# Optimization experiments

Hardware: AMD Instinct MI355X
Metric: run time of the kernel (lower is better)

## Reference

```python
import jax, jax.numpy as jnp
import numpy as np

B, N, C, H = 2, 2048, 256, 8
HD = C // H  # 32


def _pairwise_sq_dist(x, y):
    # x,y: [B,N,3] -> [B,N,N] squared euclidean distance
    x2 = jnp.sum(x * x, axis=-1)  # [B,N]
    y2 = jnp.sum(y * y, axis=-1)  # [B,N]
    xy = jnp.einsum('bnd,bmd->bnm', x, y)
    return x2[:, :, None] + y2[:, None, :] - 2.0 * xy


def setup_inputs() -> dict:
    key = jax.random.key(0)
    ks = jax.random.split(key, 12)
    s = 0.02
    return {
        'feature': jax.random.normal(ks[0], (B, N, C), jnp.float32),
        'points': jax.random.normal(ks[1], (B, N, 3), jnp.float32),
        'Wq': jax.random.normal(ks[2], (C, H * HD), jnp.float32) * s,
        'bq': jnp.zeros((H * HD,), jnp.float32),
        'Wk': jax.random.normal(ks[3], (C, H * HD), jnp.float32) * s,
        'bk': jnp.zeros((H * HD,), jnp.float32),
        'Wv': jax.random.normal(ks[4], (C, H * HD), jnp.float32) * s,
        'bv': jnp.zeros((H * HD,), jnp.float32),
        'Wo': jax.random.normal(ks[5], (H * HD, C), jnp.float32) * s,
        'bo': jnp.zeros((C,), jnp.float32),
        'ln_g': jnp.ones((C,), jnp.float32),
        'ln_b': jnp.zeros((C,), jnp.float32),
    }


def reference(feature, points, Wq, bq, Wk, bk, Wv, bv, Wo, bo, ln_g, ln_b):
    xyz = points[..., 0:3]
    dist = _pairwise_sq_dist(xyz, xyz)  # [B,N,N] geometric bias

    q = (feature @ Wq + bq).reshape(B, N, H, HD)
    k = (feature @ Wk + bk).reshape(B, N, H, HD)
    v = (feature @ Wv + bv).reshape(B, N, H, HD)

    # distance-biased multi-head attention (Geoglobal_FPT)
    logits = jnp.einsum('bnhd,bmhd->bhnm', q, k) / jnp.sqrt(jnp.float32(HD))
    logits = logits - dist[:, None, :, :]  # closer points attend more
    attn = jax.nn.softmax(logits, axis=-1)
    out = jnp.einsum('bhnm,bmhd->bnhd', attn, v).reshape(B, N, H * HD)
    out = out @ Wo + bo

    # residual + post-LayerNorm
    f = feature + out
    mu = jnp.mean(f, axis=-1, keepdims=True)
    var = jnp.mean(jnp.square(f - mu), axis=-1, keepdims=True)
    f = (f - mu) * jax.lax.rsqrt(var + 1e-5) * ln_g + ln_b
    return f
```

## Files before the change

### kernel.cpp

```cpp
#include <hip/hip_runtime.h>
#include <hip/hip_bf16.h>

#define B_ 2
#define N_ 2048
#define C_ 256
#define H_ 8
#define HD_ 32

typedef __bf16 bhalf;
typedef bhalf bhalf8 __attribute__((ext_vector_type(8)));
typedef bhalf bhalf4 __attribute__((ext_vector_type(4)));
typedef float floatx4 __attribute__((ext_vector_type(4)));
typedef short short4v __attribute__((ext_vector_type(4)));

__device__ __forceinline__ floatx4 mfma16x16x16bf16(bhalf4 a, bhalf4 b, floatx4 c) {
#if __has_builtin(__builtin_amdgcn_mfma_f32_16x16x16_bf16)
    return __builtin_amdgcn_mfma_f32_16x16x16_bf16(a, b, c, 0, 0, 0);
#else
    return __builtin_amdgcn_mfma_f32_16x16x16bf16_1k(
        __builtin_bit_cast(short4v, a), __builtin_bit_cast(short4v, b), c, 0, 0, 0);
#endif
}

__global__ __launch_bounds__(256) void prep_w(
    const float* __restrict__ Wq, const float* __restrict__ Wk,
    const float* __restrict__ Wv, const float* __restrict__ Wo,
    bhalf* __restrict__ Wtb)
{
    __shared__ float T[64][65];
    const float* W = blockIdx.y == 0 ? Wq : (blockIdx.y == 1 ? Wk : (blockIdx.y == 2 ? Wv : Wo));
    bhalf* dst = Wtb + (size_t)blockIdx.y * (C_ * C_);
    const int kt = (blockIdx.x >> 2) * 64, nt = (blockIdx.x & 3) * 64;
    const int t = threadIdx.x;
    const int c4 = (t & 15) * 4;
#pragma unroll
    for (int i = 0; i < 4; ++i) {
        const int r = (t >> 4) + i * 16;
        const float4 w = *(const float4*)&W[(kt + r) * C_ + nt + c4];
        T[r][c4 + 0] = w.x; T[r][c4 + 1] = w.y; T[r][c4 + 2] = w.z; T[r][c4 + 3] = w.w;
    }
    __syncthreads();
#pragma unroll
    for (int i = 0; i < 4; ++i) {
        const int n = (t >> 4) + i * 16;
        bhalf4 o;
        o[0] = (bhalf)T[c4 + 0][n]; o[1] = (bhalf)T[c4 + 1][n];
        o[2] = (bhalf)T[c4 + 2][n]; o[3] = (bhalf)T[c4 + 3][n];
        *(bhalf4*)&dst[(nt + n) * C_ + kt + c4] = o;
    }
}

__global__ __launch_bounds__(256) void prep_ext(
    const float* __restrict__ pts, bhalf* __restrict__ qext, bhalf* __restrict__ kext)
{
    const int i = blockIdx.x * 256 + threadIdx.x;
    const float x = pts[i * 3 + 0], y = pts[i * 3 + 1], z = pts[i * 3 + 2];
    const float nn = x * x + y * y + z * z;
    const bhalf hi = (bhalf)nn;
    const bhalf lo = (bhalf)(nn - (float)hi);
    bhalf8 qe, ke;
    qe[0] = (bhalf)(2.f * x); qe[1] = (bhalf)(2.f * y); qe[2] = (bhalf)(2.f * z);
    qe[3] = (bhalf)(-(float)hi); qe[4] = (bhalf)(-(float)lo);
    qe[5] = (bhalf)1.f; qe[6] = (bhalf)1.f; qe[7] = (bhalf)0.f;
    ke[0] = (bhalf)x; ke[1] = (bhalf)y; ke[2] = (bhalf)z;
    ke[3] = (bhalf)1.f; ke[4] = (bhalf)1.f;
    ke[5] = (bhalf)(-(float)hi); ke[6] = (bhalf)(-(float)lo); ke[7] = (bhalf)0.f;
    *(bhalf8*)&qext[(size_t)i * 8] = qe;
    *(bhalf8*)&kext[(size_t)i * 8] = ke;
}

__global__ __launch_bounds__(256) void qkv_gemm(
    const float* __restrict__ feat, const bhalf* __restrict__ Wtb,
    const float* __restrict__ bq, const float* __restrict__ bk,
    const float* __restrict__ bv,
    bhalf* __restrict__ qs, bhalf* __restrict__ kg, bhalf* __restrict__ vt)
{
    __shared__ __align__(16) bhalf Alds[64][72];
    __shared__ __align__(16) bhalf Blds[64][72];

    const int tid = threadIdx.x;
    const int wave = tid >> 6, lane = tid & 63;
    const int quad = lane >> 4, l16 = lane & 15;
    const int m0 = blockIdx.x * 64;
    const int which = blockIdx.y >> 2;
    const int n0 = (blockIdx.y & 3) * 64;
    const bhalf* Wt = Wtb + (size_t)which * (C_ * C_);
    const float* bias = which == 0 ? bq : (which == 1 ? bk : bv);

    const floatx4 zacc = {0.f, 0.f, 0.f, 0.f};
    floatx4 acc[4];
#pragma unroll
    for (int f = 0; f < 4; ++f) acc[f] = zacc;

    const int ar = tid >> 2, aseg = tid & 3;

    for (int kc = 0; kc < C_; kc += 64) {
        __syncthreads();
        {
            const float* fp = &feat[(m0 + ar) * C_ + kc + aseg * 16];
            const float4 a0 = *(const float4*)(fp);
            const float4 a1 = *(const float4*)(fp + 4);
            const float4 a2 = *(const float4*)(fp + 8);
            const float4 a3 = *(const float4*)(fp + 12);
            bhalf8 v0, v1;
            v0[0] = (bhalf)a0.x; v0[1] = (bhalf)a0.y; v0[2] = (bhalf)a0.z; v0[3] = (bhalf)a0.w;
            v0[4] = (bhalf)a1.x; v0[5] = (bhalf)a1.y; v0[6] = (bhalf)a1.z; v0[7] = (bhalf)a1.w;
            v1[0] = (bhalf)a2.x; v1[1] = (bhalf)a2.y; v1[2] = (bhalf)a2.z; v1[3] = (bhalf)a2.w;
            v1[4] = (bhalf)a3.x; v1[5] = (bhalf)a3.y; v1[6] = (bhalf)a3.z; v1[7] = (bhalf)a3.w;
            *(bhalf8*)&Alds[ar][aseg * 16] = v0;
            *(bhalf8*)&Alds[ar][aseg * 16 + 8] = v1;
            const bhalf* wp = &Wt[(n0 + ar) * C_ + kc + aseg * 16];
            *(bhalf8*)&Blds[ar][aseg * 16] = *(const bhalf8*)(wp);
            *(bhalf8*)&Blds[ar][aseg * 16 + 8] = *(const bhalf8*)(wp + 8);
        }
        __syncthreads();
        const bhalf8 af0 = *(const bhalf8*)&Alds[wave * 16 + l16][quad * 8];
        const bhalf8 af1 = *(const bhalf8*)&Alds[wave * 16 + l16][32 + quad * 8];
#pragma unroll
        for (int f = 0; f < 4; ++f) {
            const bhalf8 b0 = *(const bhalf8*)&Blds[f * 16 + l16][quad * 8];
            const bhalf8 b1 = *(const bhalf8*)&Blds[f * 16 + l16][32 + quad * 8];
            acc[f] = __builtin_amdgcn_mfma_f32_16x16x32_bf16(af0, b0, acc[f], 0, 0, 0);
            acc[f] = __builtin_amdgcn_mfma_f32_16x16x32_bf16(af1, b1, acc[f], 0, 0, 0);
        }
    }

    const float scale = 0.17677669529663687f;
#pragma unroll
    for (int f = 0; f < 4; ++f) {
        const int cg = n0 + f * 16 + l16;
        const float bi = bias[cg];
        const int hh = cg >> 5, dd = cg & 31;
#pragma unroll
        for (int r = 0; r < 4; ++r) {
            const int m = m0 + wave * 16 + quad * 4 + r;
            const int bb = m >> 11, nn = m & (N_ - 1);
            const float val = acc[f][r] + bi;
            if (which == 0) {
                qs[((size_t)(bb * H_ + hh) * N_ + nn) * HD_ + dd] = (bhalf)(val * scale);
            } else if (which == 1) {
                kg[((size_t)(bb * H_ + hh) * N_ + nn) * HD_ + dd] = (bhalf)val;
            } else {
                vt[(((size_t)(bb * H_ + hh) * (N_ / 64) + (nn >> 6)) * HD_ + dd) * 64 + (nn & 63)] = (bhalf)val;
            }
        }
    }
}

__global__ __launch_bounds__(256) void attn_kernel(
    const bhalf* __restrict__ qs, const bhalf* __restrict__ kg,
    const bhalf* __restrict__ vt, const bhalf* __restrict__ qext,
    const bhalf* __restrict__ kext,
    bhalf* __restrict__ po, float* __restrict__ pl, int spbits)
{
    __shared__ __align__(16) bhalf Ks[64][40];
    __shared__ __align__(16) bhalf Vts[32][72];

    const int tid = threadIdx.x;
    const int wave = tid >> 6, lane = tid & 63;
    const int quad = lane >> 4, l16 = lane & 15;
    const int n0 = blockIdx.x * 64;
    const int h = blockIdx.y;
    const int sp = blockIdx.z & ((1 << spbits) - 1);
    const int b = blockIdx.z >> spbits;
    const int bh = b * H_ + h;

    const int qrow = n0 + wave * 16 + l16;
    const bhalf8 bq_ = *(const bhalf8*)&qs[((size_t)bh * N_ + qrow) * HD_ + quad * 8];
    bhalf8 zv8;
#pragma unroll
    for (int j = 0; j < 8; ++j) zv8[j] = (bhalf)0.f;
    const bhalf8 bqe = (quad == 0)
        ? *(const bhalf8*)&qext[(size_t)(b * N_ + qrow) * 8] : zv8;

    const floatx4 zacc = {0.f, 0.f, 0.f, 0.f};
    floatx4 o0 = zacc, o1 = zacc;
    float ls = 0.f;

    const int skey = tid >> 2, sseg = tid & 3;
    const int vd = tid >> 3, vks = tid & 7;
    const int iters = (N_ >> spbits) / 64;
    const int mbase = sp * (N_ >> spbits);

    for (int it = 0; it < iters; ++it) {
        const int m0 = mbase + it * 64;
        __syncthreads();
        *(bhalf8*)&Ks[skey][sseg * 8] =
            *(const bhalf8*)&kg[((size_t)bh * N_ + m0 + skey) * HD_ + sseg * 8];
        *(bhalf8*)&Vts[vd][vks * 8] =
            *(const bhalf8*)&vt[(((size_t)bh * (N_ / 64) + (m0 >> 6)) * HD_ + vd) * 64 + vks * 8];
        __syncthreads();

#pragma unroll
        for (int mt = 0; mt < 4; ++mt) {
            const bhalf8 ak_ = *(const bhalf8*)&Ks[mt * 16 + l16][quad * 8];
            floatx4 st = __builtin_amdgcn_mfma_f32_16x16x32_bf16(ak_, bq_, zacc, 0, 0, 0);
            const bhalf8 ake = (quad == 0)
                ? *(const bhalf8*)&kext[(size_t)(b * N_ + m0 + mt * 16 + l16) * 8] : zv8;
            st = __builtin_amdgcn_mfma_f32_16x16x32_bf16(ake, bqe, st, 0, 0, 0);
            bhalf4 pt;
#pragma unroll
            for (int r = 0; r < 4; ++r) {
                const float p = __expf(st[r]);
                ls += p;
                pt[r] = (bhalf)p;
            }
            const bhalf4 av0 = *(const bhalf4*)&Vts[l16][mt * 16 + quad * 4];
            const bhalf4 av1 = *(const bhalf4*)&Vts[16 + l16][mt * 16 + quad * 4];
            o0 = mfma16x16x16bf16(av0, pt, o0);
            o1 = mfma16x16x16bf16(av1, pt, o1);
        }
    }

    ls += __shfl_xor(ls, 16);
    ls += __shfl_xor(ls, 32);

    const size_t pobase = (size_t)sp * ((size_t)B_ * H_ * N_ * HD_) + (size_t)bh * N_ * HD_;
    bhalf4 w0, w1;
#pragma unroll
    for (int r = 0; r < 4; ++r) { w0[r] = (bhalf)o0[r]; w1[r] = (bhalf)o1[r]; }
    *(bhalf4*)&po[pobase + (size_t)qrow * HD_ + quad * 4] = w0;
    *(bhalf4*)&po[pobase + (size_t)qrow * HD_ + 16 + quad * 4] = w1;
    if (lane < 16)
        pl[(size_t)sp * (B_ * H_ * N_) + (size_t)bh * N_ + qrow] = ls;
}

__global__ __launch_bounds__(256) void outln_gemm(
    const bhalf* __restrict__ po, const float* __restrict__ pl,
    const bhalf* __restrict__ Wot, const float* __restrict__ bo,
    const float* __restrict__ feat, const float* __restrict__ g,
    const float* __restrict__ bb, float* __restrict__ out, int splits)
{
    __shared__ __align__(16) bhalf Alds[16][264];
    __shared__ __align__(16) bhalf Blds[256][40];
    __shared__ float rden[16][8];
    __shared__ float wsum[4][16][2];
    __shared__ float stats[16][2];

    const int tid = threadIdx.x;
    const int wave = tid >> 6, lane = tid & 63;
    const int quad = lane >> 4, l16 = lane & 15;
    const int row0 = blockIdx.x * 16;

    if (tid < 128) {
        const int m = tid >> 3, hh = tid & 7;
        const int grow = row0 + m;
        const int b = grow >> 11, n = grow & (N_ - 1);
        float den = 0.f;
        for (int sp = 0; sp < splits; ++sp)
            den += pl[(size_t)sp * (B_ * H_ * N_) + (size_t)(b * H_ + hh) * N_ + n];
        rden[m][hh] = 1.f / den;
    }
    __syncthreads();

    {
        const int m = tid >> 4, seg = tid & 15;
        const int hh = seg >> 1, d0 = (seg & 1) * 16;
        const int grow = row0 + m;
        const int b = grow >> 11, n = grow & (N_ - 1);
        const size_t idx = ((size_t)(b * H_ + hh) * N_ + n) * HD_ + d0;
        float num[16];
#pragma unroll
        for (int j = 0; j < 16; ++j) num[j] = 0.f;
        for (int sp = 0; sp < splits; ++sp) {
            const bhalf8 p0 = *(const bhalf8*)&po[(size_t)sp * ((size_t)B_ * H_ * N_ * HD_) + idx];
            const bhalf8 p1 = *(const bhalf8*)&po[(size_t)sp * ((size_t)B_ * H_ * N_ * HD_) + idx + 8];
#pragma unroll
            for (int j = 0; j < 8; ++j) { num[j] += (float)p0[j]; num[8 + j] += (float)p1[j]; }
        }
        const float r = rden[m][hh];
        bhalf8 a0, a1;
#pragma unroll
        for (int j = 0; j < 8; ++j) { a0[j] = (bhalf)(num[j] * r); a1[j] = (bhalf)(num[8 + j] * r); }
        *(bhalf8*)&Alds[m][seg * 16] = a0;
        *(bhalf8*)&Alds[m][seg * 16 + 8] = a1;
    }

    const floatx4 zacc = {0.f, 0.f, 0.f, 0.f};
    floatx4 acc[4];
#pragma unroll
    for (int f = 0; f < 4; ++f) acc[f] = zacc;

    for (int kc = 0; kc < C_; kc += 32) {
        __syncthreads();
        {
            const bhalf* wp = &Wot[tid * C_ + kc];
            *(bhalf8*)&Blds[tid][0]  = *(const bhalf8*)(wp);
            *(bhalf8*)&Blds[tid][8]  = *(const bhalf8*)(wp + 8);
            *(bhalf8*)&Blds[tid][16] = *(const bhalf8*)(wp + 16);
            *(bhalf8*)&Blds[tid][24] = *(const bhalf8*)(wp + 24);
        }
        __syncthreads();
        const bhalf8 af = *(const bhalf8*)&Alds[l16][kc + quad * 8];
#pragma unroll
        for (int f = 0; f < 4; ++f) {
            const bhalf8 bfr = *(const bhalf8*)&Blds[wave * 64 + f * 16 + l16][quad * 8];
            acc[f] = __builtin_amdgcn_mfma_f32_16x16x32_bf16(af, bfr, acc[f], 0, 0, 0);
        }
    }

    float fv[4][4];
    float s1[4] = {0.f, 0.f, 0.f, 0.f}, s2[4] = {0.f, 0.f, 0.f, 0.f};
#pragma unroll
    for (int f = 0; f < 4; ++f) {
        const int col = wave * 64 + f * 16 + l16;
        const float bic = bo[col];
#pragma unroll
        for (int r = 0; r < 4; ++r) {
            const int m = quad * 4 + r;
            const float x = acc[f][r] + bic + feat[(row0 + m) * C_ + col];
            fv[f][r] = x;
            s1[r] += x; s2[r] += x * x;
        }
    }
#pragma unroll
    for (int r = 0; r < 4; ++r) {
        for (int o = 1; o < 16; o <<= 1) {
            s1[r] += __shfl_xor(s1[r], o);
            s2[r] += __shfl_xor(s2[r], o);
        }
    }
    if (l16 == 0) {
#pragma unroll
        for (int r = 0; r < 4; ++r) {
            wsum[wave][quad * 4 + r][0] = s1[r];
            wsum[wave][quad * 4 + r][1] = s2[r];
        }
    }
    __syncthreads();
    if (tid < 16) {
        float a = 0.f, bsq = 0.f;
#pragma unroll
        for (int w = 0; w < 4; ++w) { a += wsum[w][tid][0]; bsq += wsum[w][tid][1]; }
        const float mu = a * (1.f / C_);
        const float var = bsq * (1.f / C_) - mu * mu;
        stats[tid][0] = mu;
        stats[tid][1] = rsqrtf(var + 1e-5f);
    }
    __syncthreads();
#pragma unroll
    for (int f = 0; f < 4; ++f) {
        const int col = wave * 64 + f * 16 + l16;
        const float gc = g[col], bc = bb[col];
#pragma unroll
        for (int r = 0; r < 4; ++r) {
            const int m = quad * 4 + r;
            out[(row0 + m) * C_ + col] = (fv[f][r] - stats[m][0]) * stats[m][1] * gc + bc;
        }
    }
}

extern "C" void kernel_launch(void* const* d_in, const int* in_sizes, int n_in,
                              void* d_out, int out_size, void* d_ws, size_t ws_size,
                              hipStream_t stream) {
    const float* feat = (const float*)d_in[0];
    const float* pts  = (const float*)d_in[1];
    const float* Wq   = (const float*)d_in[2];
    const float* bq   = (const float*)d_in[3];
    const float* Wk   = (const float*)d_in[4];
    const float* bk   = (const float*)d_in[5];
    const float* Wv   = (const float*)d_in[6];
    const float* bv   = (const float*)d_in[7];
    const float* Wo   = (const float*)d_in[8];
    const float* bo   = (const float*)d_in[9];
    const float* lng  = (const float*)d_in[10];
    const float* lnb  = (const float*)d_in[11];

    char* w = (char*)d_ws;
    bhalf* Wtb  = (bhalf*)(w);
    bhalf* qs   = (bhalf*)(w + 524288);
    bhalf* kg   = (bhalf*)(w + 2621440);
    bhalf* vtp  = (bhalf*)(w + 4718592);
    bhalf* qext = (bhalf*)(w + 6815744);
    bhalf* kext = (bhalf*)(w + 6881280);
    float* pl   = (float*)(w + 6946816);
    bhalf* po   = (bhalf*)(w + 7471104);

    const int spbits = (ws_size >= 15859712u) ? 2 : 1;
    const int splits = 1 << spbits;

    prep_w<<<dim3(16, 4), 256, 0, stream>>>(Wq, Wk, Wv, Wo, Wtb);
    prep_ext<<<B_ * N_ / 256, 256, 0, stream>>>(pts, qext, kext);
    qkv_gemm<<<dim3(B_ * N_ / 64, 12), 256, 0, stream>>>(
        feat, Wtb, bq, bk, bv, qs, kg, vtp);
    attn_kernel<<<dim3(N_ / 64, H_, B_ << spbits), 256, 0, stream>>>(
        qs, kg, vtp, qext, kext, po, pl, spbits);
    outln_gemm<<<B_ * N_ / 16, 256, 0, stream>>>(
        po, pl, Wtb + 3 * (C_ * C_), bo, feat, lng, lnb, (float*)d_out, splits);
}
```

Baseline: 132.3 us.

## Merge prep kernels, pre-convert features to bf16, double-buffer LDS in all GEMM loops

Folds the weight transpose, point-extension and a new feature fp32-to-bf16 conversion into one prep launch. The QKV GEMM now reads bf16 features, uses 32-row tiles for twice as many blocks, and double-buffers LDS with register prefetch. The attention and output GEMM loops get the same double-buffered prefetch, and attention stages kext in LDS instead of reading it from global memory per tile. This trades extra LDS and registers plus an extra feature buffer round trip for fewer launches and fewer barrier stalls.

```diff
diff --git a/kernel.cpp b/kernel.cpp
--- a/kernel.cpp
+++ b/kernel.cpp
@@ -22,118 +22,130 @@
 #endif
 }
 
-__global__ __launch_bounds__(256) void prep_w(
+__global__ __launch_bounds__(256) void prep_all(
     const float* __restrict__ Wq, const float* __restrict__ Wk,
     const float* __restrict__ Wv, const float* __restrict__ Wo,
-    bhalf* __restrict__ Wtb)
+    const float* __restrict__ pts, const float* __restrict__ feat,
+    bhalf* __restrict__ Wtb, bhalf* __restrict__ qext,
+    bhalf* __restrict__ kext, bhalf* __restrict__ fb)
 {
     __shared__ float T[64][65];
-    const float* W = blockIdx.y == 0 ? Wq : (blockIdx.y == 1 ? Wk : (blockIdx.y == 2 ? Wv : Wo));
-    bhalf* dst = Wtb + (size_t)blockIdx.y * (C_ * C_);
-    const int kt = (blockIdx.x >> 2) * 64, nt = (blockIdx.x & 3) * 64;
+    const int bx = blockIdx.x;
     const int t = threadIdx.x;
-    const int c4 = (t & 15) * 4;
-#pragma unroll
-    for (int i = 0; i < 4; ++i) {
-        const int r = (t >> 4) + i * 16;
-        const float4 w = *(const float4*)&W[(kt + r) * C_ + nt + c4];
-        T[r][c4 + 0] = w.x; T[r][c4 + 1] = w.y; T[r][c4 + 2] = w.z; T[r][c4 + 3] = w.w;
-    }
-    __syncthreads();
-#pragma unroll
-    for (int i = 0; i < 4; ++i) {
-        const int n = (t >> 4) + i * 16;
+    if (bx < 64) {
+        const int wsel = bx >> 4;
+        const float* W = wsel == 0 ? Wq : (wsel == 1 ? Wk : (wsel == 2 ? Wv : Wo));
+        bhalf* dst = Wtb + (size_t)wsel * (C_ * C_);
+        const int tile = bx & 15;
+        const int kt = (tile >> 2) * 64, nt = (tile & 3) * 64;
+        const int c4 = (t & 15) * 4;
+#pragma unroll
+        for (int i = 0; i < 4; ++i) {
+            const int r = (t >> 4) + i * 16;
+            const float4 w = *(const float4*)&W[(kt + r) * C_ + nt + c4];
+            T[r][c4 + 0] = w.x; T[r][c4 + 1] = w.y; T[r][c4 + 2] = w.z; T[r][c4 + 3] = w.w;
+        }
+        __syncthreads();
+#pragma unroll
+        for (int i = 0; i < 4; ++i) {
+            const int n = (t >> 4) + i * 16;
+            bhalf4 o;
+            o[0] = (bhalf)T[c4 + 0][n]; o[1] = (bhalf)T[c4 + 1][n];
+            o[2] = (bhalf)T[c4 + 2][n]; o[3] = (bhalf)T[c4 + 3][n];
+            *(bhalf4*)&dst[(nt + n) * C_ + kt + c4] = o;
+        }
+    } else if (bx < 80) {
+        const int i = (bx - 64) * 256 + t;
+        const float x = pts[i * 3 + 0], y = pts[i * 3 + 1], z = pts[i * 3 + 2];
+        const float nn = x * x + y * y + z * z;
+        const bhalf hi = (bhalf)nn;
+        const bhalf lo = (bhalf)(nn - (float)hi);
+        bhalf8 qe, ke;
+        qe[0] = (bhalf)(2.f * x); qe[1] = (bhalf)(2.f * y); qe[2] = (bhalf)(2.f * z);
+        qe[3] = (bhalf)(-(float)hi); qe[4] = (bhalf)(-(float)lo);
+        qe[5] = (bhalf)1.f; qe[6] = (bhalf)1.f; qe[7] = (bhalf)0.f;
+        ke[0] = (bhalf)x; ke[1] = (bhalf)y; ke[2] = (bhalf)z;
+        ke[3] = (bhalf)1.f; ke[4] = (bhalf)1.f;
+        ke[5] = (bhalf)(-(float)hi); ke[6] = (bhalf)(-(float)lo); ke[7] = (bhalf)0.f;
+        *(bhalf8*)&qext[(size_t)i * 8] = qe;
+        *(bhalf8*)&kext[(size_t)i * 8] = ke;
+    } else {
+        const int idx = ((bx - 80) * 256 + t) * 4;
+        const float4 f = *(const float4*)&feat[idx];
         bhalf4 o;
-        o[0] = (bhalf)T[c4 + 0][n]; o[1] = (bhalf)T[c4 + 1][n];
-        o[2] = (bhalf)T[c4 + 2][n]; o[3] = (bhalf)T[c4 + 3][n];
-        *(bhalf4*)&dst[(nt + n) * C_ + kt + c4] = o;
-    }
-}
-
-__global__ __launch_bounds__(256) void prep_ext(
-    const float* __restrict__ pts, bhalf* __restrict__ qext, bhalf* __restrict__ kext)
-{
-    const int i = blockIdx.x * 256 + threadIdx.x;
-    const float x = pts[i * 3 + 0], y = pts[i * 3 + 1], z = pts[i * 3 + 2];
-    const float nn = x * x + y * y + z * z;
-    const bhalf hi = (bhalf)nn;
-    const bhalf lo = (bhalf)(nn - (float)hi);
-    bhalf8 qe, ke;
-    qe[0] = (bhalf)(2.f * x); qe[1] = (bhalf)(2.f * y); qe[2] = (bhalf)(2.f * z);
-    qe[3] = (bhalf)(-(float)hi); qe[4] = (bhalf)(-(float)lo);
-    qe[5] = (bhalf)1.f; qe[6] = (bhalf)1.f; qe[7] = (bhalf)0.f;
-    ke[0] = (bhalf)x; ke[1] = (bhalf)y; ke[2] = (bhalf)z;
-    ke[3] = (bhalf)1.f; ke[4] = (bhalf)1.f;
-    ke[5] = (bhalf)(-(float)hi); ke[6] = (bhalf)(-(float)lo); ke[7] = (bhalf)0.f;
-    *(bhalf8*)&qext[(size_t)i * 8] = qe;
-    *(bhalf8*)&kext[(size_t)i * 8] = ke;
+        o[0] = (bhalf)f.x; o[1] = (bhalf)f.y; o[2] = (bhalf)f.z; o[3] = (bhalf)f.w;
+        *(bhalf4*)&fb[idx] = o;
+    }
 }
 
 __global__ __launch_bounds__(256) void qkv_gemm(
-    const float* __restrict__ feat, const bhalf* __restrict__ Wtb,
+    const bhalf* __restrict__ fb, const bhalf* __restrict__ Wtb,
     const float* __restrict__ bq, const float* __restrict__ bk,
     const float* __restrict__ bv,
     bhalf* __restrict__ qs, bhalf* __restrict__ kg, bhalf* __restrict__ vt)
 {
-    __shared__ __align__(16) bhalf Alds[64][72];
-    __shared__ __align__(16) bhalf Blds[64][72];
+    __shared__ __align__(16) bhalf Alds[2][32][72];
+    __shared__ __align__(16) bhalf Blds[2][64][72];
 
     const int tid = threadIdx.x;
     const int wave = tid >> 6, lane = tid & 63;
     const int quad = lane >> 4, l16 = lane & 15;
-    const int m0 = blockIdx.x * 64;
+    const int m0 = blockIdx.x * 32;
     const int which = blockIdx.y >> 2;
     const int n0 = (blockIdx.y & 3) * 64;
     const bhalf* Wt = Wtb + (size_t)which * (C_ * C_);
+    const int mw = (wave & 1) * 16;
+    const int cw = (wave >> 1) * 32;
+
+    const floatx4 zacc = {0.f, 0.f, 0.f, 0.f};
+    floatx4 acc[2] = {zacc, zacc};
+
+    const int arow = tid >> 3, aoff = (tid & 7) * 8;
+    const int brow = tid >> 2, boff = (tid & 3) * 16;
+
+    bhalf8 ra  = *(const bhalf8*)&fb[(m0 + arow) * C_ + aoff];
+    bhalf8 rb0 = *(const bhalf8*)&Wt[(n0 + brow) * C_ + boff];
+    bhalf8 rb1 = *(const bhalf8*)&Wt[(n0 + brow) * C_ + boff + 8];
+    *(bhalf8*)&Alds[0][arow][aoff] = ra;
+    *(bhalf8*)&Blds[0][brow][boff] = rb0;
+    *(bhalf8*)&Blds[0][brow][boff + 8] = rb1;
+
+    int cur = 0;
+    for (int kci = 0; kci < 4; ++kci) {
+        __syncthreads();
+        if (kci < 3) {
+            const int kc = (kci + 1) * 64;
+            ra  = *(const bhalf8*)&fb[(m0 + arow) * C_ + kc + aoff];
+            rb0 = *(const bhalf8*)&Wt[(n0 + brow) * C_ + kc + boff];
+            rb1 = *(const bhalf8*)&Wt[(n0 + brow) * C_ + kc + boff + 8];
+        }
+        const bhalf8 a0 = *(const bhalf8*)&Alds[cur][mw + l16][quad * 8];
+        const bhalf8 a1 = *(const bhalf8*)&Alds[cur][mw + l16][32 + quad * 8];
+#pragma unroll
+        for (int f = 0; f < 2; ++f) {
+            const bhalf8 b0 = *(const bhalf8*)&Blds[cur][cw + f * 16 + l16][quad * 8];
+            const bhalf8 b1 = *(const bhalf8*)&Blds[cur][cw + f * 16 + l16][32 + quad * 8];
+            acc[f] = __builtin_amdgcn_mfma_f32_16x16x32_bf16(a0, b0, acc[f], 0, 0, 0);
+            acc[f] = __builtin_amdgcn_mfma_f32_16x16x32_bf16(a1, b1, acc[f], 0, 0, 0);
+        }
+        if (kci < 3) {
+            *(bhalf8*)&Alds[cur ^ 1][arow][aoff] = ra;
+            *(bhalf8*)&Blds[cur ^ 1][brow][boff] = rb0;
+            *(bhalf8*)&Blds[cur ^ 1][brow][boff + 8] = rb1;
+        }
+        cur ^= 1;
+    }
+
+    const float scale = 0.17677669529663687f;
     const float* bias = which == 0 ? bq : (which == 1 ? bk : bv);
-
-    const floatx4 zacc = {0.f, 0.f, 0.f, 0.f};
-    floatx4 acc[4];
-#pragma unroll
-    for (int f = 0; f < 4; ++f) acc[f] = zacc;
-
-    const int ar = tid >> 2, aseg = tid & 3;
-
-    for (int kc = 0; kc < C_; kc += 64) {
-        __syncthreads();
-        {
-            const float* fp = &feat[(m0 + ar) * C_ + kc + aseg * 16];
-            const float4 a0 = *(const float4*)(fp);
-            const float4 a1 = *(const float4*)(fp + 4);
-            const float4 a2 = *(const float4*)(fp + 8);
-            const float4 a3 = *(const float4*)(fp + 12);
-            bhalf8 v0, v1;
-            v0[0] = (bhalf)a0.x; v0[1] = (bhalf)a0.y; v0[2] = (bhalf)a0.z; v0[3] = (bhalf)a0.w;
-            v0[4] = (bhalf)a1.x; v0[5] = (bhalf)a1.y; v0[6] = (bhalf)a1.z; v0[7] = (bhalf)a1.w;
-            v1[0] = (bhalf)a2.x; v1[1] = (bhalf)a2.y; v1[2] = (bhalf)a2.z; v1[3] = (bhalf)a2.w;
-            v1[4] = (bhalf)a3.x; v1[5] = (bhalf)a3.y; v1[6] = (bhalf)a3.z; v1[7] = (bhalf)a3.w;
-            *(bhalf8*)&Alds[ar][aseg * 16] = v0;
-            *(bhalf8*)&Alds[ar][aseg * 16 + 8] = v1;
-            const bhalf* wp = &Wt[(n0 + ar) * C_ + kc + aseg * 16];
-            *(bhalf8*)&Blds[ar][aseg * 16] = *(const bhalf8*)(wp);
-            *(bhalf8*)&Blds[ar][aseg * 16 + 8] = *(const bhalf8*)(wp + 8);
-        }
-        __syncthreads();
-        const bhalf8 af0 = *(const bhalf8*)&Alds[wave * 16 + l16][quad * 8];
-        const bhalf8 af1 = *(const bhalf8*)&Alds[wave * 16 + l16][32 + quad * 8];
-#pragma unroll
-        for (int f = 0; f < 4; ++f) {
-            const bhalf8 b0 = *(const bhalf8*)&Blds[f * 16 + l16][quad * 8];
-            const bhalf8 b1 = *(const bhalf8*)&Blds[f * 16 + l16][32 + quad * 8];
-            acc[f] = __builtin_amdgcn_mfma_f32_16x16x32_bf16(af0, b0, acc[f], 0, 0, 0);
-            acc[f] = __builtin_amdgcn_mfma_f32_16x16x32_bf16(af1, b1, acc[f], 0, 0, 0);
-        }
-    }
-
-    const float scale = 0.17677669529663687f;
-#pragma unroll
-    for (int f = 0; f < 4; ++f) {
-        const int cg = n0 + f * 16 + l16;
+#pragma unroll
+    for (int f = 0; f < 2; ++f) {
+        const int cg = n0 + cw + f * 16 + l16;
         const float bi = bias[cg];
         const int hh = cg >> 5, dd = cg & 31;
 #pragma unroll
         for (int r = 0; r < 4; ++r) {
-            const int m = m0 + wave * 16 + quad * 4 + r;
+            const int m = m0 + mw + quad * 4 + r;
             const int bb = m >> 11, nn = m & (N_ - 1);
             const float val = acc[f][r] + bi;
             if (which == 0) {
@@ -153,8 +165,9 @@
     const bhalf* __restrict__ kext,
     bhalf* __restrict__ po, float* __restrict__ pl, int spbits)
 {
-    __shared__ __align__(16) bhalf Ks[64][40];
-    __shared__ __align__(16) bhalf Vts[32][72];
+    __shared__ __align__(16) bhalf Ks[2][64][40];
+    __shared__ __align__(16) bhalf Vts[2][32][72];
+    __shared__ __align__(16) bhalf Kes[2][64][8];
 
     const int tid = threadIdx.x;
     const int wave = tid >> 6, lane = tid & 63;
@@ -179,24 +192,33 @@
 
     const int skey = tid >> 2, sseg = tid & 3;
     const int vd = tid >> 3, vks = tid & 7;
+    const int ekey = tid >> 1, eoff = (tid & 1) * 4;
     const int iters = (N_ >> spbits) / 64;
     const int mbase = sp * (N_ >> spbits);
 
+    bhalf8 rk = *(const bhalf8*)&kg[((size_t)bh * N_ + mbase + skey) * HD_ + sseg * 8];
+    bhalf8 rv = *(const bhalf8*)&vt[(((size_t)bh * (N_ / 64) + (mbase >> 6)) * HD_ + vd) * 64 + vks * 8];
+    bhalf4 re;
+    if (tid < 128) re = *(const bhalf4*)&kext[(size_t)(b * N_ + mbase + ekey) * 8 + eoff];
+    *(bhalf8*)&Ks[0][skey][sseg * 8] = rk;
+    *(bhalf8*)&Vts[0][vd][vks * 8] = rv;
+    if (tid < 128) *(bhalf4*)&Kes[0][ekey][eoff] = re;
+
+    int cur = 0;
     for (int it = 0; it < iters; ++it) {
-        const int m0 = mbase + it * 64;
         __syncthreads();
-        *(bhalf8*)&Ks[skey][sseg * 8] =
-            *(const bhalf8*)&kg[((size_t)bh * N_ + m0 + skey) * HD_ + sseg * 8];
-        *(bhalf8*)&Vts[vd][vks * 8] =
-            *(const bhalf8*)&vt[(((size_t)bh * (N_ / 64) + (m0 >> 6)) * HD_ + vd) * 64 + vks * 8];
-        __syncthreads();
-
+        if (it + 1 < iters) {
+            const int m1 = mbase + (it + 1) * 64;
+            rk = *(const bhalf8*)&kg[((size_t)bh * N_ + m1 + skey) * HD_ + sseg * 8];
+            rv = *(const bhalf8*)&vt[(((size_t)bh * (N_ / 64) + (m1 >> 6)) * HD_ + vd) * 64 + vks * 8];
+            if (tid < 128) re = *(const bhalf4*)&kext[(size_t)(b * N_ + m1 + ekey) * 8 + eoff];
+        }
 #pragma unroll
         for (int mt = 0; mt < 4; ++mt) {
-            const bhalf8 ak_ = *(const bhalf8*)&Ks[mt * 16 + l16][quad * 8];
+            const bhalf8 ak_ = *(const bhalf8*)&Ks[cur][mt * 16 + l16][quad * 8];
             floatx4 st = __builtin_amdgcn_mfma_f32_16x16x32_bf16(ak_, bq_, zacc, 0, 0, 0);
             const bhalf8 ake = (quad == 0)
-                ? *(const bhalf8*)&kext[(size_t)(b * N_ + m0 + mt * 16 + l16) * 8] : zv8;
+                ? *(const bhalf8*)&Kes[cur][mt * 16 + l16][0] : zv8;
             st = __builtin_amdgcn_mfma_f32_16x16x32_bf16(ake, bqe, st, 0, 0, 0);
             bhalf4 pt;
 #pragma unroll
@@ -205,11 +227,17 @@
                 ls += p;
                 pt[r] = (bhalf)p;
             }
-            const bhalf4 av0 = *(const bhalf4*)&Vts[l16][mt * 16 + quad * 4];
-            const bhalf4 av1 = *(const bhalf4*)&Vts[16 + l16][mt * 16 + quad * 4];
+            const bhalf4 av0 = *(const bhalf4*)&Vts[cur][l16][mt * 16 + quad * 4];
+            const bhalf4 av1 = *(const bhalf4*)&Vts[cur][16 + l16][mt * 16 + quad * 4];
             o0 = mfma16x16x16bf16(av0, pt, o0);
             o1 = mfma16x16x16bf16(av1, pt, o1);
         }
+        if (it + 1 < iters) {
+            *(bhalf8*)&Ks[cur ^ 1][skey][sseg * 8] = rk;
+            *(bhalf8*)&Vts[cur ^ 1][vd][vks * 8] = rv;
+            if (tid < 128) *(bhalf4*)&Kes[cur ^ 1][ekey][eoff] = re;
+        }
+        cur ^= 1;
     }
 
     ls += __shfl_xor(ls, 16);
@@ -232,7 +260,7 @@
     const float* __restrict__ bb, float* __restrict__ out, int splits)
 {
     __shared__ __align__(16) bhalf Alds[16][264];
-    __shared__ __align__(16) bhalf Blds[256][40];
+    __shared__ __align__(16) bhalf Blds[2][256][40];
     __shared__ float rden[16][8];
     __shared__ float wsum[4][16][2];
     __shared__ float stats[16][2];
@@ -281,22 +309,38 @@
 #pragma unroll
     for (int f = 0; f < 4; ++f) acc[f] = zacc;
 
-    for (int kc = 0; kc < C_; kc += 32) {
+    bhalf8 rb0 = *(const bhalf8*)&Wot[tid * C_ + 0];
+    bhalf8 rb1 = *(const bhalf8*)&Wot[tid * C_ + 8];
+    bhalf8 rb2 = *(const bhalf8*)&Wot[tid * C_ + 16];
+    bhalf8 rb3 = *(const bhalf8*)&Wot[tid * C_ + 24];
+    *(bhalf8*)&Blds[0][tid][0]  = rb0;
+    *(bhalf8*)&Blds[0][tid][8]  = rb1;
+    *(bhalf8*)&Blds[0][tid][16] = rb2;
+    *(bhalf8*)&Blds[0][tid][24] = rb3;
+
+    int cur = 0;
+    for (int kci = 0; kci < 8; ++kci) {
         __syncthreads();
-        {
-            const bhalf* wp = &Wot[tid * C_ + kc];
-            *(bhalf8*)&Blds[tid][0]  = *(const bhalf8*)(wp);
-            *(bhalf8*)&Blds[tid][8]  = *(const bhalf8*)(wp + 8);
-            *(bhalf8*)&Blds[tid][16] = *(const bhalf8*)(wp + 16);
-            *(bhalf8*)&Blds[tid][24] = *(const bhalf8*)(wp + 24);
-        }
-        __syncthreads();
-        const bhalf8 af = *(const bhalf8*)&Alds[l16][kc + quad * 8];
+        if (kci < 7) {
+            const bhalf* wp = &Wot[tid * C_ + (kci + 1) * 32];
+            rb0 = *(const bhalf8*)(wp);
+            rb1 = *(const bhalf8*)(wp + 8);
+            rb2 = *(const bhalf8*)(wp + 16);
+            rb3 = *(const bhalf8*)(wp + 24);
+        }
+        const bhalf8 af = *(const bhalf8*)&Alds[l16][kci * 32 + quad * 8];
 #pragma unroll
         for (int f = 0; f < 4; ++f) {
-            const bhalf8 bfr = *(const bhalf8*)&Blds[wave * 64 + f * 16 + l16][quad * 8];
+            const bhalf8 bfr = *(const bhalf8*)&Blds[cur][wave * 64 + f * 16 + l16][quad * 8];
             acc[f] = __builtin_amdgcn_mfma_f32_16x16x32_bf16(af, bfr, acc[f], 0, 0, 0);
         }
+        if (kci < 7) {
+            *(bhalf8*)&Blds[cur ^ 1][tid][0]  = rb0;
+            *(bhalf8*)&Blds[cur ^ 1][tid][8]  = rb1;
+            *(bhalf8*)&Blds[cur ^ 1][tid][16] = rb2;
+            *(bhalf8*)&Blds[cur ^ 1][tid][24] = rb3;
+        }
+        cur ^= 1;
     }
 
     float fv[4][4];
@@ -368,21 +412,22 @@
 
     char* w = (char*)d_ws;
     bhalf* Wtb  = (bhalf*)(w);
-    bhalf* qs   = (bhalf*)(w + 524288);
-    bhalf* kg   = (bhalf*)(w + 2621440);
-    bhalf* vtp  = (bhalf*)(w + 4718592);
-    bhalf* qext = (bhalf*)(w + 6815744);
-    bhalf* kext = (bhalf*)(w + 6881280);
-    float* pl   = (float*)(w + 6946816);
-    bhalf* po   = (bhalf*)(w + 7471104);
-
-    const int spbits = (ws_size >= 15859712u) ? 2 : 1;
+    bhalf* fb   = (bhalf*)(w + 524288);
+    bhalf* qs   = (bhalf*)(w + 2621440);
+    bhalf* kg   = (bhalf*)(w + 4718592);
+    bhalf* vtp  = (bhalf*)(w + 6815744);
+    bhalf* qext = (bhalf*)(w + 8912896);
+    bhalf* kext = (bhalf*)(w + 8978432);
+    float* pl   = (float*)(w + 9043968);
+    bhalf* po   = (bhalf*)(w + 9568256);
+
+    const int spbits = (ws_size >= 17956864u) ? 2 : 1;
     const int splits = 1 << spbits;
 
-    prep_w<<<dim3(16, 4), 256, 0, stream>>>(Wq, Wk, Wv, Wo, Wtb);
-    prep_ext<<<B_ * N_ / 256, 256, 0, stream>>>(pts, qext, kext);
-    qkv_gemm<<<dim3(B_ * N_ / 64, 12), 256, 0, stream>>>(
-        feat, Wtb, bq, bk, bv, qs, kg, vtp);
+    prep_all<<<80 + B_ * N_ * C_ / 1024, 256, 0, stream>>>(
+        Wq, Wk, Wv, Wo, pts, feat, Wtb, qext, kext, fb);
+    qkv_gemm<<<dim3(B_ * N_ / 32, 12), 256, 0, stream>>>(
+        fb, Wtb, bq, bk, bv, qs, kg, vtp);
     attn_kernel<<<dim3(N_ / 64, H_, B_ << spbits), 256, 0, stream>>>(
         qs, kg, vtp, qext, kext, po, pl, spbits);
     outln_gemm<<<B_ * N_ / 16, 256, 0, stream>>>(
```

After: 125.9 us. 4.9% less time.
